# Performance work log

Measured on AMD Instinct MI355X. Metric: run time of the kernel, lower is better.

Reference implementation:

```python
import jax, jax.numpy as jnp
import numpy as np

N, E, D = 10000, 160000, 256
EPS = 1e-5


def layer_norm(x, gamma, beta):
    mu = jnp.mean(x, axis=-1, keepdims=True)
    var = jnp.var(x, axis=-1, keepdims=True)
    return (x - mu) * jax.lax.rsqrt(var + EPS) * gamma + beta


def mlp(x, w1, b1, w2, b2):
    return jax.nn.relu(x @ w1 + b1) @ w2 + b2


def setup_inputs() -> dict:
    key = jax.random.key(0)
    ks = jax.random.split(key, 16)
    s = lambda fan_in: 1.0 / np.sqrt(fan_in)
    inp = {
        'x': jax.random.normal(ks[0], (N, D), jnp.float32),
        'edge_index': jax.random.randint(ks[1], (2, E), 0, N, jnp.int64),
        'edge_attr': jax.random.normal(ks[2], (E, D), jnp.float32),
        # edge MLP: in 3D=768 -> hidden 2D=512 -> out D=256, then LN
        'e_w1': jax.random.uniform(ks[3], (3 * D, 2 * D), jnp.float32, -s(3 * D), s(3 * D)),
        'e_b1': jnp.zeros((2 * D,), jnp.float32),
        'e_w2': jax.random.uniform(ks[4], (2 * D, D), jnp.float32, -s(2 * D), s(2 * D)),
        'e_b2': jnp.zeros((D,), jnp.float32),
        'e_g': jnp.ones((D,), jnp.float32),
        'e_beta': jnp.zeros((D,), jnp.float32),
        # node MLP: in 2D=512 -> hidden 2D=512 -> out D=256, then LN
        'n_w1': jax.random.uniform(ks[5], (2 * D, 2 * D), jnp.float32, -s(2 * D), s(2 * D)),
        'n_b1': jnp.zeros((2 * D,), jnp.float32),
        'n_w2': jax.random.uniform(ks[6], (2 * D, D), jnp.float32, -s(2 * D), s(2 * D)),
        'n_b2': jnp.zeros((D,), jnp.float32),
        'n_g': jnp.ones((D,), jnp.float32),
        'n_beta': jnp.zeros((D,), jnp.float32),
    }
    return inp


def reference(x, edge_index, edge_attr, e_w1, e_b1, e_w2, e_b2, e_g, e_beta,
              n_w1, n_b1, n_w2, n_b2, n_g, n_beta):
    i, j = edge_index[0], edge_index[1]
    # Edge processor: gather, concat, MLP + LN, residual
    h = jnp.concatenate([x[i], x[j], edge_attr], axis=-1)  # [E, 3D]
    new_edge = edge_attr + layer_norm(mlp(h, e_w1, e_b1, e_w2, e_b2), e_g, e_beta)
    # Node processor: scatter-add over j, concat, MLP + LN, residual
    agg = jax.ops.segment_sum(new_edge, j, num_segments=x.shape[0])  # [N, D]
    hn = jnp.concatenate([x, agg], axis=-1)  # [N, 2D]
    new_x = x + layer_norm(mlp(hn, n_w1, n_b1, n_w2, n_b2), n_g, n_beta)
    return new_x, new_edge
```

## Files before the change

### kernel.cpp

```cpp
#include <hip/hip_runtime.h>

#define NNODE 10000
#define NEDGE 160000
#define DD 256

using f32x4  = __attribute__((ext_vector_type(4))) float;
using bf16x8 = __attribute__((ext_vector_type(8))) short;
using u32x4  = __attribute__((ext_vector_type(4))) unsigned;

__device__ inline short f2bf(float f) {
  unsigned u = __float_as_uint(f);
  unsigned r = (u + 0x7fffu + ((u >> 16) & 1u)) >> 16;
  return (short)(unsigned short)r;
}

__device__ inline unsigned pkbf(float a, float b) {
  unsigned r;
  asm("v_cvt_pk_bf16_f32 %0, %1, %2" : "=v"(r) : "v"(a), "v"(b));
  return r;
}

__global__ void cast_x_kernel(const float* __restrict__ x, short* __restrict__ xb, int total) {
  int i = blockIdx.x * 256 + threadIdx.x;
  if (i < total) xb[i] = f2bf(x[i]);
}

__global__ void pack_w_kernel(const float* __restrict__ w, short* __restrict__ p, int K, int N) {
  int idx = blockIdx.x * 256 + threadIdx.x;
  if (idx >= K * N) return;
  int k = idx / N, n = idx - k * N;
  p[(size_t)(k >> 3) * N * 8 + (size_t)n * 8 + (k & 7)] = f2bf(w[idx]);
}

__global__ void hist_kernel(const int* __restrict__ ei, int* __restrict__ deg) {
  int e = blockIdx.x * 256 + threadIdx.x;
  if (e < NEDGE) {
    int j = ei[NEDGE + e]; j = min(max(j, 0), NNODE - 1);
    atomicAdd(&deg[j], 1);
  }
}

__global__ void scan_kernel(const int* __restrict__ deg, int* __restrict__ row_start) {
  __shared__ int part[256];
  int t = threadIdx.x;
  const int CH = 40;
  int base = t * CH;
  int s = 0;
  for (int i = 0; i < CH; i++) {
    int idx = base + i;
    s += (idx < NNODE) ? deg[idx] : 0;
  }
  part[t] = s;
  __syncthreads();
  for (int off = 1; off < 256; off <<= 1) {
    int v = (t >= off) ? part[t - off] : 0;
    __syncthreads();
    part[t] += v;
    __syncthreads();
  }
  int run = (t == 0) ? 0 : part[t - 1];
  for (int i = 0; i < CH; i++) {
    int idx = base + i;
    if (idx < NNODE) { row_start[idx] = run; run += deg[idx]; }
  }
  if (t == 255) row_start[NNODE] = part[255];
}

__global__ void scatter_kernel(const int* __restrict__ ei, const int* __restrict__ row_start,
                               int* __restrict__ cursor, int* __restrict__ csr) {
  int e = blockIdx.x * 256 + threadIdx.x;
  if (e < NEDGE) {
    int j = ei[NEDGE + e]; j = min(max(j, 0), NNODE - 1);
    int p = atomicAdd(&cursor[j], 1);
    csr[row_start[j] + p] = e;
  }
}

__global__ __launch_bounds__(256) void agg_kernel(const float* __restrict__ out_e,
                                                  const int* __restrict__ row_start,
                                                  const int* __restrict__ csr,
                                                  short* __restrict__ aggb) {
  int node = blockIdx.x * 4 + (threadIdx.x >> 6);
  int lane = threadIdx.x & 63;
  if (node >= NNODE) return;
  int rs = row_start[node], re = row_start[node + 1];
  float4 acc = {0.f, 0.f, 0.f, 0.f};
  for (int k = rs; k < re; k++) {
    int eid = csr[k];
    float4 v = *(const float4*)(out_e + (size_t)eid * DD + lane * 4);
    acc.x += v.x; acc.y += v.y; acc.z += v.z; acc.w += v.w;
  }
  short4 o;
  o.x = f2bf(acc.x); o.y = f2bf(acc.y); o.z = f2bf(acc.z); o.w = f2bf(acc.w);
  *(short4*)(aggb + (size_t)node * DD + lane * 4) = o;
}

template<int MODE>
__global__ __launch_bounds__(256, 2)
void fused_mlp(const float* __restrict__ x,
               const short* __restrict__ xb,
               const int*   __restrict__ ei,
               const float* __restrict__ ea,
               const short* __restrict__ aggb,
               const short* __restrict__ w1p,
               const float* __restrict__ b1,
               const short* __restrict__ w2p,
               const float* __restrict__ b2,
               const float* __restrict__ gam,
               const float* __restrict__ bet,
               float*       __restrict__ out)
{
  constexpr int K1 = (MODE == 0) ? 768 : 512;
  constexpr int NSTEP = K1 / 64;
  constexpr int HP = 520;

  __shared__ __align__(16) short hid[64 * HP];
  __shared__ float pS[4][64];
  __shared__ float pQ[4][64];

  const int tid  = threadIdx.x;
  const int lane = tid & 63;
  const int wid  = tid >> 6;
  const int m0   = blockIdx.x * 64;
  const int lhi  = lane >> 4;
  const int llo  = lane & 15;

  const short* pI[4]; const short* pJ[4]; const float* pE[4];
  #pragma unroll
  for (int mf = 0; mf < 4; mf++) {
    int rowg = m0 + mf * 16 + llo;
    if (MODE == 0) {
      int ii = ei[rowg];         ii = min(max(ii, 0), NNODE - 1);
      int jj = ei[NEDGE + rowg]; jj = min(max(jj, 0), NNODE - 1);
      pI[mf] = xb + (size_t)ii * DD;
      pJ[mf] = xb + (size_t)jj * DD;
      pE[mf] = ea + (size_t)rowg * DD;
    } else {
      int rr = min(rowg, NNODE - 1);
      pI[mf] = xb + (size_t)rr * DD;
      pJ[mf] = aggb + (size_t)rr * DD;
      pE[mf] = nullptr;
    }
  }

  f32x4 acc1[4][8] = {};
  const bf16x8* bp1 = (const bf16x8*)w1p;
  const int bcol1 = wid * 128 + llo;

  #pragma unroll
  for (int s = 0; s < NSTEP; s++) {
    #pragma unroll
    for (int kk = 0; kk < 64; kk += 32) {
      const int ko = s * 64 + kk + lhi * 8;
      bf16x8 a[4];
      #pragma unroll
      for (int mf = 0; mf < 4; mf++) {
        if (MODE == 0) {
          if (s < 4)      a[mf] = *(const bf16x8*)(pI[mf] + ko);
          else if (s < 8) a[mf] = *(const bf16x8*)(pJ[mf] + (ko - 256));
          else {
            const float* fp = pE[mf] + (ko - 512);
            float4 u0 = *(const float4*)fp;
            float4 u1 = *(const float4*)(fp + 4);
            u32x4 q = { pkbf(u0.x, u0.y), pkbf(u0.z, u0.w),
                        pkbf(u1.x, u1.y), pkbf(u1.z, u1.w) };
            a[mf] = __builtin_bit_cast(bf16x8, q);
          }
        } else {
          if (s < 4) a[mf] = *(const bf16x8*)(pI[mf] + ko);
          else       a[mf] = *(const bf16x8*)(pJ[mf] + (ko - 256));
        }
      }
      const bf16x8* bbase = bp1 + (size_t)(((s * 64 + kk) >> 3) + lhi) * 512 + bcol1;
      #pragma unroll
      for (int nf = 0; nf < 8; nf++) {
        bf16x8 b = bbase[nf * 16];
        #pragma unroll
        for (int mf = 0; mf < 4; mf++)
          acc1[mf][nf] = __builtin_amdgcn_mfma_f32_16x16x32_bf16(a[mf], b, acc1[mf][nf], 0, 0, 0);
      }
    }
  }

  #pragma unroll
  for (int nf = 0; nf < 8; nf++) {
    int col = wid * 128 + nf * 16 + llo;
    float bb = b1[col];
    #pragma unroll
    for (int mf = 0; mf < 4; mf++) {
      #pragma unroll
      for (int r = 0; r < 4; r++) {
        float v = acc1[mf][nf][r] + bb;
        v = v > 0.f ? v : 0.f;
        hid[(mf * 16 + lhi * 4 + r) * HP + col] = f2bf(v);
      }
    }
  }
  __syncthreads();

  f32x4 acc2[4][4] = {};
  const bf16x8* bp2 = (const bf16x8*)w2p;
  const int bcol2 = wid * 64 + llo;
  #pragma unroll
  for (int kk = 0; kk < 512; kk += 32) {
    bf16x8 a[4];
    #pragma unroll
    for (int mf = 0; mf < 4; mf++)
      a[mf] = *(const bf16x8*)(hid + (mf * 16 + llo) * HP + kk + lhi * 8);
    const bf16x8* bbase = bp2 + (size_t)((kk >> 3) + lhi) * 256 + bcol2;
    #pragma unroll
    for (int nf = 0; nf < 4; nf++) {
      bf16x8 b = bbase[nf * 16];
      #pragma unroll
      for (int mf = 0; mf < 4; mf++)
        acc2[mf][nf] = __builtin_amdgcn_mfma_f32_16x16x32_bf16(a[mf], b, acc2[mf][nf], 0, 0, 0);
    }
  }

  float bb2[4], gg[4], be[4];
  #pragma unroll
  for (int nf = 0; nf < 4; nf++) {
    int col = bcol2 + nf * 16;
    bb2[nf] = b2[col]; gg[nf] = gam[col]; be[nf] = bet[col];
  }
  #pragma unroll
  for (int mf = 0; mf < 4; mf++)
    #pragma unroll
    for (int nf = 0; nf < 4; nf++)
      #pragma unroll
      for (int r = 0; r < 4; r++)
        acc2[mf][nf][r] += bb2[nf];

  float S[4][4], Q[4][4];
  #pragma unroll
  for (int mf = 0; mf < 4; mf++) {
    #pragma unroll
    for (int r = 0; r < 4; r++) {
      float s = 0.f, q = 0.f;
      #pragma unroll
      for (int nf = 0; nf < 4; nf++) {
        float v = acc2[mf][nf][r];
        s += v; q += v * v;
      }
      S[mf][r] = s; Q[mf][r] = q;
    }
  }
  #pragma unroll
  for (int m = 1; m <= 8; m <<= 1) {
    #pragma unroll
    for (int mf = 0; mf < 4; mf++)
      #pragma unroll
      for (int r = 0; r < 4; r++) {
        S[mf][r] += __shfl_xor(S[mf][r], m);
        Q[mf][r] += __shfl_xor(Q[mf][r], m);
      }
  }
  if (llo == 0) {
    #pragma unroll
    for (int mf = 0; mf < 4; mf++)
      #pragma unroll
      for (int r = 0; r < 4; r++) {
        int row = mf * 16 + lhi * 4 + r;
        pS[wid][row] = S[mf][r];
        pQ[wid][row] = Q[mf][r];
      }
  }
  __syncthreads();

  float mu[4][4], rsv[4][4];
  #pragma unroll
  for (int mf = 0; mf < 4; mf++) {
    #pragma unroll
    for (int r = 0; r < 4; r++) {
      int row = mf * 16 + lhi * 4 + r;
      float s = pS[0][row] + pS[1][row] + pS[2][row] + pS[3][row];
      float q = pQ[0][row] + pQ[1][row] + pQ[2][row] + pQ[3][row];
      float m_ = s * (1.f / 256.f);
      mu[mf][r]  = m_;
      rsv[mf][r] = rsqrtf(q * (1.f / 256.f) - m_ * m_ + 1e-5f);
    }
  }

  const float* resb = (MODE == 0) ? ea : x;
  #pragma unroll
  for (int mf = 0; mf < 4; mf++) {
    #pragma unroll
    for (int r = 0; r < 4; r++) {
      int grow = m0 + mf * 16 + lhi * 4 + r;
      if (MODE == 1 && grow >= NNODE) continue;
      const float* rp = resb + (size_t)grow * DD + bcol2;
      float*       op = out  + (size_t)grow * DD + bcol2;
      #pragma unroll
      for (int nf = 0; nf < 4; nf++) {
        float v = (acc2[mf][nf][r] - mu[mf][r]) * rsv[mf][r] * gg[nf] + be[nf] + rp[nf * 16];
        op[nf * 16] = v;
      }
    }
  }
}

extern "C" void kernel_launch(void* const* d_in, const int* in_sizes, int n_in,
                              void* d_out, int out_size, void* d_ws, size_t ws_size,
                              hipStream_t stream) {
  const float* x      = (const float*)d_in[0];
  const int*   ei     = (const int*)  d_in[1];
  const float* ea     = (const float*)d_in[2];
  const float* e_w1   = (const float*)d_in[3];
  const float* e_b1   = (const float*)d_in[4];
  const float* e_w2   = (const float*)d_in[5];
  const float* e_b2   = (const float*)d_in[6];
  const float* e_g    = (const float*)d_in[7];
  const float* e_beta = (const float*)d_in[8];
  const float* n_w1   = (const float*)d_in[9];
  const float* n_b1   = (const float*)d_in[10];
  const float* n_w2   = (const float*)d_in[11];
  const float* n_b2   = (const float*)d_in[12];
  const float* n_g    = (const float*)d_in[13];
  const float* n_beta = (const float*)d_in[14];

  float* out_x = (float*)d_out;
  float* out_e = (float*)d_out + (size_t)NNODE * DD;

  char* w = (char*)d_ws;
  short* xb   = (short*)(w);
  short* ew1p = (short*)(w + 5120000);
  short* nw1p = (short*)(w + 5906432);
  short* ew2p = (short*)(w + 6430720);
  short* nw2p = (short*)(w + 6692864);
  short* aggb = (short*)(w + 6955008);
  int*   deg  = (int*)  (w + 12075008);
  int*   cur  = (int*)  (w + 12115968);
  int*   rs   = (int*)  (w + 12156928);
  int*   csr  = (int*)  (w + 12197904);

  hipMemsetAsync(deg, 0, 81920, stream);

  cast_x_kernel<<<(NNODE * DD + 255) / 256, 256, 0, stream>>>(x, xb, NNODE * DD);
  pack_w_kernel<<<(768 * 512 + 255) / 256, 256, 0, stream>>>(e_w1, ew1p, 768, 512);
  pack_w_kernel<<<(512 * 512 + 255) / 256, 256, 0, stream>>>(n_w1, nw1p, 512, 512);
  pack_w_kernel<<<(512 * 256 + 255) / 256, 256, 0, stream>>>(e_w2, ew2p, 512, 256);
  pack_w_kernel<<<(512 * 256 + 255) / 256, 256, 0, stream>>>(n_w2, nw2p, 512, 256);

  hist_kernel<<<(NEDGE + 255) / 256, 256, 0, stream>>>(ei, deg);
  scan_kernel<<<1, 256, 0, stream>>>(deg, rs);
  scatter_kernel<<<(NEDGE + 255) / 256, 256, 0, stream>>>(ei, rs, cur, csr);

  fused_mlp<0><<<NEDGE / 64, 256, 0, stream>>>(x, xb, ei, ea, aggb,
                                               ew1p, e_b1, ew2p, e_b2, e_g, e_beta, out_e);
  agg_kernel<<<(NNODE + 3) / 4, 256, 0, stream>>>(out_e, rs, csr, aggb);
  fused_mlp<1><<<(NNODE + 63) / 64, 256, 0, stream>>>(x, xb, ei, ea, aggb,
                                                      nw1p, n_b1, nw2p, n_b2, n_g, n_beta, out_x);
}
```

Baseline: 532.6 us.

## Stage A tiles in LDS via async loads and split hidden into two halves

The fused MLP now stages the gathered activation tile into a double-buffered, XOR-swizzled LDS buffer using global_load_lds, instead of each wave loading A fragments directly from global memory. The hidden layer is computed in two 256-column halves, each fed straight into the second GEMM. This halves the acc1 registers and the hid LDS footprint, which allows raising launch bounds to 3 blocks per CU. The cost is that the first GEMM's A operand is re-staged twice and more barriers are added.

```diff
diff --git a/kernel.cpp b/kernel.cpp
--- a/kernel.cpp
+++ b/kernel.cpp
@@ -96,7 +96,7 @@
 }
 
 template<int MODE>
-__global__ __launch_bounds__(256, 2)
+__global__ __launch_bounds__(256, 3)
 void fused_mlp(const float* __restrict__ x,
                const short* __restrict__ xb,
                const int*   __restrict__ ei,
@@ -110,13 +110,14 @@
                const float* __restrict__ bet,
                float*       __restrict__ out)
 {
-  constexpr int K1 = (MODE == 0) ? 768 : 512;
-  constexpr int NSTEP = K1 / 64;
-  constexpr int HP = 520;
-
+  constexpr int K1  = (MODE == 0) ? 768 : 512;
+  constexpr int NST = K1 / 64;
+  constexpr int HP  = 264;
+
+  __shared__ __align__(16) short abuf[2][4096];
   __shared__ __align__(16) short hid[64 * HP];
-  __shared__ float pS[4][64];
-  __shared__ float pQ[4][64];
+  __shared__ int idxi[64], idxj[64];
+  __shared__ float pS[4][64], pQ[4][64];
 
   const int tid  = threadIdx.x;
   const int lane = tid & 63;
@@ -125,98 +126,140 @@
   const int lhi  = lane >> 4;
   const int llo  = lane & 15;
 
-  const short* pI[4]; const short* pJ[4]; const float* pE[4];
-  #pragma unroll
-  for (int mf = 0; mf < 4; mf++) {
-    int rowg = m0 + mf * 16 + llo;
-    if (MODE == 0) {
-      int ii = ei[rowg];         ii = min(max(ii, 0), NNODE - 1);
-      int jj = ei[NEDGE + rowg]; jj = min(max(jj, 0), NNODE - 1);
-      pI[mf] = xb + (size_t)ii * DD;
-      pJ[mf] = xb + (size_t)jj * DD;
-      pE[mf] = ea + (size_t)rowg * DD;
+  if (MODE == 0) {
+    if (tid < 64) {
+      int a = ei[m0 + tid];
+      int b = ei[NEDGE + m0 + tid];
+      idxi[tid] = min(max(a, 0), NNODE - 1);
+      idxj[tid] = min(max(b, 0), NNODE - 1);
+    }
+    __syncthreads();
+  }
+
+  const int row0 = tid >> 3;
+  const int row1 = 32 + (tid >> 3);
+  const int es0 = (((tid & 7) ^ (row0 & 7)) * 8);
+  const int es1 = (((tid & 7) ^ (row1 & 7)) * 8);
+  int offI0, offI1, offJ0, offJ1, offE0, offE1;
+  if (MODE == 0) {
+    offI0 = idxi[row0] * 512 + es0 * 2;  offI1 = idxi[row1] * 512 + es1 * 2;
+    offJ0 = idxj[row0] * 512 + es0 * 2;  offJ1 = idxj[row1] * 512 + es1 * 2;
+    offE0 = (m0 + row0) * 1024 + es0 * 4; offE1 = (m0 + row1) * 1024 + es1 * 4;
+  } else {
+    int r0 = min(m0 + row0, NNODE - 1), r1 = min(m0 + row1, NNODE - 1);
+    offI0 = r0 * 512 + es0 * 2;  offI1 = r1 * 512 + es1 * 2;
+    offJ0 = r0 * 512 + es0 * 2;  offJ1 = r1 * 512 + es1 * 2;
+    offE0 = 0; offE1 = 0;
+  }
+
+  auto STAGE = [&](int buf, int k0) {
+    if (MODE == 1 || k0 < 512) {
+      const char* base;
+      int o0, o1;
+      if (k0 < 256) {
+        base = (const char*)xb;
+        o0 = offI0 + k0 * 2; o1 = offI1 + k0 * 2;
+      } else {
+        base = (MODE == 0) ? (const char*)xb : (const char*)aggb;
+        o0 = offJ0 + (k0 - 256) * 2; o1 = offJ1 + (k0 - 256) * 2;
+      }
+      __builtin_amdgcn_global_load_lds((const int*)(base + o0),
+                                       (int*)&abuf[buf][wid * 512], 16, 0, 0);
+      __builtin_amdgcn_global_load_lds((const int*)(base + o1),
+                                       (int*)&abuf[buf][2048 + wid * 512], 16, 0, 0);
     } else {
-      int rr = min(rowg, NNODE - 1);
-      pI[mf] = xb + (size_t)rr * DD;
-      pJ[mf] = aggb + (size_t)rr * DD;
-      pE[mf] = nullptr;
-    }
-  }
-
-  f32x4 acc1[4][8] = {};
+      const char* eb = (const char*)ea;
+      const float4* f0 = (const float4*)(eb + offE0 + (k0 - 512) * 4);
+      const float4* f1 = (const float4*)(eb + offE1 + (k0 - 512) * 4);
+      float4 a0 = f0[0], a1 = f0[1];
+      float4 c0 = f1[0], c1 = f1[1];
+      u32x4 q0 = { pkbf(a0.x, a0.y), pkbf(a0.z, a0.w), pkbf(a1.x, a1.y), pkbf(a1.z, a1.w) };
+      u32x4 q1 = { pkbf(c0.x, c0.y), pkbf(c0.z, c0.w), pkbf(c1.x, c1.y), pkbf(c1.z, c1.w) };
+      *(u32x4*)&abuf[buf][tid * 8]        = q0;
+      *(u32x4*)&abuf[buf][2048 + tid * 8] = q1;
+    }
+  };
+
+  f32x4 acc1[4][4];
+  f32x4 acc2[4][4];
+  #pragma unroll
+  for (int a = 0; a < 4; a++)
+    #pragma unroll
+    for (int b = 0; b < 4; b++)
+      #pragma unroll
+      for (int r = 0; r < 4; r++) { acc1[a][b][r] = 0.f; acc2[a][b][r] = 0.f; }
+
   const bf16x8* bp1 = (const bf16x8*)w1p;
-  const int bcol1 = wid * 128 + llo;
-
-  #pragma unroll
-  for (int s = 0; s < NSTEP; s++) {
-    #pragma unroll
-    for (int kk = 0; kk < 64; kk += 32) {
-      const int ko = s * 64 + kk + lhi * 8;
-      bf16x8 a[4];
-      #pragma unroll
-      for (int mf = 0; mf < 4; mf++) {
-        if (MODE == 0) {
-          if (s < 4)      a[mf] = *(const bf16x8*)(pI[mf] + ko);
-          else if (s < 8) a[mf] = *(const bf16x8*)(pJ[mf] + (ko - 256));
-          else {
-            const float* fp = pE[mf] + (ko - 512);
-            float4 u0 = *(const float4*)fp;
-            float4 u1 = *(const float4*)(fp + 4);
-            u32x4 q = { pkbf(u0.x, u0.y), pkbf(u0.z, u0.w),
-                        pkbf(u1.x, u1.y), pkbf(u1.z, u1.w) };
-            a[mf] = __builtin_bit_cast(bf16x8, q);
-          }
-        } else {
-          if (s < 4) a[mf] = *(const bf16x8*)(pI[mf] + ko);
-          else       a[mf] = *(const bf16x8*)(pJ[mf] + (ko - 256));
-        }
-      }
-      const bf16x8* bbase = bp1 + (size_t)(((s * 64 + kk) >> 3) + lhi) * 512 + bcol1;
-      #pragma unroll
-      for (int nf = 0; nf < 8; nf++) {
-        bf16x8 b = bbase[nf * 16];
+  const bf16x8* bp2 = (const bf16x8*)w2p;
+  const int swz = llo & 7;
+
+  STAGE(0, 0);
+  __syncthreads();
+
+  #pragma unroll
+  for (int p = 0; p < 2; p++) {
+    #pragma unroll 2
+    for (int s = 0; s < NST; s++) {
+      if (s < NST - 1) STAGE((s + 1) & 1, (s + 1) * 64);
+      const short* ab = &abuf[s & 1][0];
+      #pragma unroll
+      for (int kk = 0; kk < 64; kk += 32) {
+        bf16x8 a[4];
+        const int seg = ((kk >> 3) + lhi) ^ swz;
         #pragma unroll
         for (int mf = 0; mf < 4; mf++)
-          acc1[mf][nf] = __builtin_amdgcn_mfma_f32_16x16x32_bf16(a[mf], b, acc1[mf][nf], 0, 0, 0);
-      }
-    }
-  }
-
-  #pragma unroll
-  for (int nf = 0; nf < 8; nf++) {
-    int col = wid * 128 + nf * 16 + llo;
-    float bb = b1[col];
-    #pragma unroll
-    for (int mf = 0; mf < 4; mf++) {
-      #pragma unroll
-      for (int r = 0; r < 4; r++) {
-        float v = acc1[mf][nf][r] + bb;
-        v = v > 0.f ? v : 0.f;
-        hid[(mf * 16 + lhi * 4 + r) * HP + col] = f2bf(v);
-      }
-    }
-  }
-  __syncthreads();
-
-  f32x4 acc2[4][4] = {};
-  const bf16x8* bp2 = (const bf16x8*)w2p;
+          a[mf] = *(const bf16x8*)(ab + (mf * 16 + llo) * 64 + seg * 8);
+        const bf16x8* bb = bp1 + (size_t)(s * 8 + (kk >> 3) + lhi) * 512
+                               + (p * 256 + wid * 64 + llo);
+        #pragma unroll
+        for (int nf = 0; nf < 4; nf++) {
+          bf16x8 b = bb[nf * 16];
+          #pragma unroll
+          for (int mf = 0; mf < 4; mf++)
+            acc1[mf][nf] = __builtin_amdgcn_mfma_f32_16x16x32_bf16(a[mf], b, acc1[mf][nf], 0, 0, 0);
+        }
+      }
+      __syncthreads();
+    }
+
+    #pragma unroll
+    for (int nf = 0; nf < 4; nf++) {
+      int col = wid * 64 + nf * 16 + llo;
+      float bb = b1[p * 256 + col];
+      #pragma unroll
+      for (int mf = 0; mf < 4; mf++) {
+        #pragma unroll
+        for (int r = 0; r < 4; r++) {
+          float v = acc1[mf][nf][r] + bb;
+          v = v > 0.f ? v : 0.f;
+          hid[(mf * 16 + lhi * 4 + r) * HP + col] = f2bf(v);
+          acc1[mf][nf][r] = 0.f;
+        }
+      }
+    }
+    __syncthreads();
+
+    if (p == 0) STAGE(0, 0);
+
+    #pragma unroll 2
+    for (int kk = 0; kk < 256; kk += 32) {
+      bf16x8 a[4];
+      #pragma unroll
+      for (int mf = 0; mf < 4; mf++)
+        a[mf] = *(const bf16x8*)(hid + (mf * 16 + llo) * HP + kk + lhi * 8);
+      const bf16x8* bb = bp2 + (size_t)(p * 32 + (kk >> 3) + lhi) * 256 + (wid * 64 + llo);
+      #pragma unroll
+      for (int nf = 0; nf < 4; nf++) {
+        bf16x8 b = bb[nf * 16];
+        #pragma unroll
+        for (int mf = 0; mf < 4; mf++)
+          acc2[mf][nf] = __builtin_amdgcn_mfma_f32_16x16x32_bf16(a[mf], b, acc2[mf][nf], 0, 0, 0);
+      }
+    }
+    __syncthreads();
+  }
+
   const int bcol2 = wid * 64 + llo;
-  #pragma unroll
-  for (int kk = 0; kk < 512; kk += 32) {
-    bf16x8 a[4];
-    #pragma unroll
-    for (int mf = 0; mf < 4; mf++)
-      a[mf] = *(const bf16x8*)(hid + (mf * 16 + llo) * HP + kk + lhi * 8);
-    const bf16x8* bbase = bp2 + (size_t)((kk >> 3) + lhi) * 256 + bcol2;
-    #pragma unroll
-    for (int nf = 0; nf < 4; nf++) {
-      bf16x8 b = bbase[nf * 16];
-      #pragma unroll
-      for (int mf = 0; mf < 4; mf++)
-        acc2[mf][nf] = __builtin_amdgcn_mfma_f32_16x16x32_bf16(a[mf], b, acc2[mf][nf], 0, 0, 0);
-    }
-  }
-
   float bb2[4], gg[4], be[4];
   #pragma unroll
   for (int nf = 0; nf < 4; nf++) {
```

Result: slower. 546.4 us (+2.6%).

## Precompute per-node first-layer projections and gather them per edge

Applied to the files above, without the earlier changes.

The first edge-MLP layer is split algebraically: x@W1a and x@W1b are computed once per node (10k rows) into a bf16 table, and each edge gathers two 512-wide rows and adds them to edge_attr@W1c. This cuts the edge GEMM K dimension from 768 to 256. It removes the redundant per-edge recomputation of node projections. Edge_attr is now staged through LDS with an XOR swizzle, and the hidden buffer is swizzled too. The cost is an extra bf16 rounding of the partial sums, a 20MB intermediate, and random gathers of 1KB rows per edge.

```diff
diff --git a/kernel.cpp b/kernel.cpp
--- a/kernel.cpp
+++ b/kernel.cpp
@@ -12,6 +12,10 @@
   unsigned u = __float_as_uint(f);
   unsigned r = (u + 0x7fffu + ((u >> 16) & 1u)) >> 16;
   return (short)(unsigned short)r;
+}
+
+__device__ inline float bf2f(short s) {
+  return __uint_as_float(((unsigned)(unsigned short)s) << 16);
 }
 
 __device__ inline unsigned pkbf(float a, float b) {
@@ -30,6 +34,23 @@
   if (idx >= K * N) return;
   int k = idx / N, n = idx - k * N;
   p[(size_t)(k >> 3) * N * 8 + (size_t)n * 8 + (k & 7)] = f2bf(w[idx]);
+}
+
+__global__ void pack_ew1_kernel(const float* __restrict__ w, short* __restrict__ w1abp,
+                                short* __restrict__ w1cp) {
+  int idx = blockIdx.x * 256 + threadIdx.x;
+  if (idx >= 768 * 512) return;
+  int k = idx >> 9, n = idx & 511;
+  short v = f2bf(w[idx]);
+  if (k < 256) {
+    w1abp[(size_t)(k >> 3) * 1024 * 8 + (size_t)n * 8 + (k & 7)] = v;
+  } else if (k < 512) {
+    int kk = k - 256;
+    w1abp[(size_t)(kk >> 3) * 1024 * 8 + (size_t)(512 + n) * 8 + (kk & 7)] = v;
+  } else {
+    int kk = k - 512;
+    w1cp[(size_t)(kk >> 3) * 512 * 8 + (size_t)n * 8 + (kk & 7)] = v;
+  }
 }
 
 __global__ void hist_kernel(const int* __restrict__ ei, int* __restrict__ deg) {
@@ -95,28 +116,284 @@
   *(short4*)(aggb + (size_t)node * DD + lane * 4) = o;
 }
 
-template<int MODE>
 __global__ __launch_bounds__(256, 2)
-void fused_mlp(const float* __restrict__ x,
-               const short* __restrict__ xb,
-               const int*   __restrict__ ei,
-               const float* __restrict__ ea,
-               const short* __restrict__ aggb,
-               const short* __restrict__ w1p,
-               const float* __restrict__ b1,
-               const short* __restrict__ w2p,
-               const float* __restrict__ b2,
-               const float* __restrict__ gam,
-               const float* __restrict__ bet,
-               float*       __restrict__ out)
+void precomp_pab(const short* __restrict__ xb, const short* __restrict__ w1abp,
+                 short* __restrict__ pab) {
+  __shared__ __align__(16) short abuf[2048 * 8];
+
+  const int tid  = threadIdx.x;
+  const int lane = tid & 63;
+  const int wid  = tid >> 6;
+  const int lhi  = lane >> 4;
+  const int llo  = lane & 15;
+  const int swz  = llo & 7;
+  const int m0   = blockIdx.x * 64;
+  const int h    = blockIdx.y;
+
+  #pragma unroll
+  for (int q = 0; q < 8; q++) {
+    int S = wid * 512 + q * 64 + lane;
+    int row = S >> 5;
+    int segp = S & 31;
+    int seg = segp ^ (row & 7);
+    int rowg = min(m0 + row, NNODE - 1);
+    __builtin_amdgcn_global_load_lds(
+        (const int*)((const char*)xb + (size_t)rowg * 512 + seg * 16),
+        (int*)(abuf + (size_t)(wid * 512 + q * 64) * 8), 16, 0, 0);
+  }
+  __syncthreads();
+
+  f32x4 acc1[4][8] = {};
+  const bf16x8* bp1 = (const bf16x8*)w1abp;
+  #pragma unroll
+  for (int kk = 0; kk < 256; kk += 32) {
+    const int ks = kk >> 3;
+    bf16x8 a[4];
+    #pragma unroll
+    for (int mf = 0; mf < 4; mf++)
+      a[mf] = *(const bf16x8*)(abuf + ((mf * 16 + llo) * 32 + ((ks + lhi) ^ swz)) * 8);
+    const bf16x8* bb = bp1 + (size_t)(ks + lhi) * 1024 + h * 512 + wid * 128 + llo;
+    #pragma unroll
+    for (int nf = 0; nf < 8; nf++) {
+      bf16x8 b = bb[nf * 16];
+      #pragma unroll
+      for (int mf = 0; mf < 4; mf++)
+        acc1[mf][nf] = __builtin_amdgcn_mfma_f32_16x16x32_bf16(a[mf], b, acc1[mf][nf], 0, 0, 0);
+    }
+  }
+
+  #pragma unroll
+  for (int mf = 0; mf < 4; mf++) {
+    #pragma unroll
+    for (int r = 0; r < 4; r++) {
+      int row = m0 + mf * 16 + lhi * 4 + r;
+      if (row < NNODE) {
+        u32x4 wv = { pkbf(acc1[mf][0][r], acc1[mf][1][r]),
+                     pkbf(acc1[mf][2][r], acc1[mf][3][r]),
+                     pkbf(acc1[mf][4][r], acc1[mf][5][r]),
+                     pkbf(acc1[mf][6][r], acc1[mf][7][r]) };
+        *(u32x4*)(pab + (size_t)row * 1024 + h * 512 + llo * 32 + wid * 8) = wv;
+      }
+    }
+  }
+}
+
+__global__ __launch_bounds__(256, 2)
+void fused_edge(const int* __restrict__ ei,
+                const float* __restrict__ ea,
+                const short* __restrict__ pab,
+                const short* __restrict__ w1cp,
+                const float* __restrict__ b1,
+                const short* __restrict__ w2p,
+                const float* __restrict__ b2,
+                const float* __restrict__ gam,
+                const float* __restrict__ bet,
+                float* __restrict__ out)
 {
-  constexpr int K1 = (MODE == 0) ? 768 : 512;
-  constexpr int NSTEP = K1 / 64;
+  __shared__ __align__(16) short hid[64 * 512];
+  __shared__ int idxi[64], idxj[64];
+  __shared__ float pS[256], pQ[256];
+
+  short* abuf = hid;
+
+  const int tid  = threadIdx.x;
+  const int lane = tid & 63;
+  const int wid  = tid >> 6;
+  const int lhi  = lane >> 4;
+  const int llo  = lane & 15;
+  const int swz  = llo & 7;
+  const int m0   = blockIdx.x * 64;
+
+  if (tid < 64) {
+    int a = ei[m0 + tid];
+    int b = ei[NEDGE + m0 + tid];
+    idxi[tid] = min(max(a, 0), NNODE - 1);
+    idxj[tid] = min(max(b, 0), NNODE - 1);
+  }
+
+  #pragma unroll
+  for (int q = 0; q < 8; q++) {
+    int S = q * 256 + tid;
+    int row = S >> 5;
+    int segp = S & 31;
+    int seg = segp ^ (row & 7);
+    const float* src = ea + (size_t)(m0 + row) * 256 + seg * 8;
+    float4 u0 = *(const float4*)src;
+    float4 u1 = *(const float4*)(src + 4);
+    u32x4 qv = { pkbf(u0.x, u0.y), pkbf(u0.z, u0.w), pkbf(u1.x, u1.y), pkbf(u1.z, u1.w) };
+    *(u32x4*)(abuf + (size_t)S * 8) = qv;
+  }
+  __syncthreads();
+
+  f32x4 acc1[4][8] = {};
+  const bf16x8* bp1 = (const bf16x8*)w1cp;
+  #pragma unroll
+  for (int kk = 0; kk < 256; kk += 32) {
+    const int ks = kk >> 3;
+    bf16x8 a[4];
+    #pragma unroll
+    for (int mf = 0; mf < 4; mf++)
+      a[mf] = *(const bf16x8*)(abuf + ((mf * 16 + llo) * 32 + ((ks + lhi) ^ swz)) * 8);
+    const bf16x8* bb = bp1 + (size_t)(ks + lhi) * 512 + wid * 128 + llo;
+    #pragma unroll
+    for (int nf = 0; nf < 8; nf++) {
+      bf16x8 b = bb[nf * 16];
+      #pragma unroll
+      for (int mf = 0; mf < 4; mf++)
+        acc1[mf][nf] = __builtin_amdgcn_mfma_f32_16x16x32_bf16(a[mf], b, acc1[mf][nf], 0, 0, 0);
+    }
+  }
+
+  #pragma unroll
+  for (int mf = 0; mf < 4; mf++) {
+    #pragma unroll
+    for (int r = 0; r < 4; r++) {
+      int row = mf * 16 + lhi * 4 + r;
+      int gi = idxi[row], gj = idxj[row];
+      bf16x8 pa = *(const bf16x8*)(pab + (size_t)gi * 1024 + llo * 32 + wid * 8);
+      bf16x8 pb = *(const bf16x8*)(pab + (size_t)gj * 1024 + 512 + llo * 32 + wid * 8);
+      #pragma unroll
+      for (int nf = 0; nf < 8; nf++)
+        acc1[mf][nf][r] += bf2f(pa[nf]) + bf2f(pb[nf]);
+    }
+  }
+  __syncthreads();
+
+  #pragma unroll
+  for (int nf = 0; nf < 8; nf++) {
+    int col = wid * 128 + nf * 16 + llo;
+    float bb = b1[col];
+    int cs = col >> 3, cl = col & 7;
+    #pragma unroll
+    for (int mf = 0; mf < 4; mf++) {
+      #pragma unroll
+      for (int r = 0; r < 4; r++) {
+        int row = mf * 16 + lhi * 4 + r;
+        float v = acc1[mf][nf][r] + bb;
+        v = v > 0.f ? v : 0.f;
+        hid[row * 512 + ((cs ^ (row & 7)) * 8) + cl] = f2bf(v);
+      }
+    }
+  }
+  __syncthreads();
+
+  f32x4 acc2[4][4] = {};
+  const bf16x8* bp2 = (const bf16x8*)w2p;
+  const int bcol2 = wid * 64 + llo;
+  #pragma unroll
+  for (int kk = 0; kk < 512; kk += 32) {
+    const int ks = kk >> 3;
+    bf16x8 a[4];
+    #pragma unroll
+    for (int mf = 0; mf < 4; mf++) {
+      int row = mf * 16 + llo;
+      a[mf] = *(const bf16x8*)(hid + row * 512 + (((ks + lhi) ^ swz) * 8));
+    }
+    const bf16x8* bb = bp2 + (size_t)(ks + lhi) * 256 + bcol2;
+    #pragma unroll
+    for (int nf = 0; nf < 4; nf++) {
+      bf16x8 b = bb[nf * 16];
+      #pragma unroll
+      for (int mf = 0; mf < 4; mf++)
+        acc2[mf][nf] = __builtin_amdgcn_mfma_f32_16x16x32_bf16(a[mf], b, acc2[mf][nf], 0, 0, 0);
+    }
+  }
+
+  float bb2[4], gg[4], be[4];
+  #pragma unroll
+  for (int nf = 0; nf < 4; nf++) {
+    int col = bcol2 + nf * 16;
+    bb2[nf] = b2[col]; gg[nf] = gam[col]; be[nf] = bet[col];
+  }
+  #pragma unroll
+  for (int mf = 0; mf < 4; mf++)
+    #pragma unroll
+    for (int nf = 0; nf < 4; nf++)
+      #pragma unroll
+      for (int r = 0; r < 4; r++)
+        acc2[mf][nf][r] += bb2[nf];
+
+  float S[4][4], Q[4][4];
+  #pragma unroll
+  for (int mf = 0; mf < 4; mf++) {
+    #pragma unroll
+    for (int r = 0; r < 4; r++) {
+      float s = 0.f, q = 0.f;
+      #pragma unroll
+      for (int nf = 0; nf < 4; nf++) {
+        float v = acc2[mf][nf][r];
+        s += v; q += v * v;
+      }
+      S[mf][r] = s; Q[mf][r] = q;
+    }
+  }
+  #pragma unroll
+  for (int m = 1; m <= 8; m <<= 1) {
+    #pragma unroll
+    for (int mf = 0; mf < 4; mf++)
+      #pragma unroll
+      for (int r = 0; r < 4; r++) {
+        S[mf][r] += __shfl_xor(S[mf][r], m);
+        Q[mf][r] += __shfl_xor(Q[mf][r], m);
+      }
+  }
+  if (llo == 0) {
+    #pragma unroll
+    for (int mf = 0; mf < 4; mf++)
+      #pragma unroll
+      for (int r = 0; r < 4; r++) {
+        int row = mf * 16 + lhi * 4 + r;
+        pS[wid * 64 + row] = S[mf][r];
+        pQ[wid * 64 + row] = Q[mf][r];
+      }
+  }
+  __syncthreads();
+
+  float mu[4][4], rsv[4][4];
+  #pragma unroll
+  for (int mf = 0; mf < 4; mf++) {
+    #pragma unroll
+    for (int r = 0; r < 4; r++) {
+      int row = mf * 16 + lhi * 4 + r;
+      float s = pS[row] + pS[64 + row] + pS[128 + row] + pS[192 + row];
+      float q = pQ[row] + pQ[64 + row] + pQ[128 + row] + pQ[192 + row];
+      float m_ = s * (1.f / 256.f);
+      mu[mf][r]  = m_;
+      rsv[mf][r] = rsqrtf(q * (1.f / 256.f) - m_ * m_ + 1e-5f);
+    }
+  }
+
+  #pragma unroll
+  for (int mf = 0; mf < 4; mf++) {
+    #pragma unroll
+    for (int r = 0; r < 4; r++) {
+      int grow = m0 + mf * 16 + lhi * 4 + r;
+      const float* rp = ea  + (size_t)grow * DD + bcol2;
+      float*       op = out + (size_t)grow * DD + bcol2;
+      #pragma unroll
+      for (int nf = 0; nf < 4; nf++) {
+        float v = (acc2[mf][nf][r] - mu[mf][r]) * rsv[mf][r] * gg[nf] + be[nf] + rp[nf * 16];
+        op[nf * 16] = v;
+      }
+    }
+  }
+}
+
+__global__ __launch_bounds__(256, 2)
+void fused_node(const float* __restrict__ x,
+                const short* __restrict__ xb,
+                const short* __restrict__ aggb,
+                const short* __restrict__ w1p,
+                const float* __restrict__ b1,
+                const short* __restrict__ w2p,
+                const float* __restrict__ b2,
+                const float* __restrict__ gam,
+                const float* __restrict__ bet,
+                float* __restrict__ out)
+{
   constexpr int HP = 520;
-
   __shared__ __align__(16) short hid[64 * HP];
-  __shared__ float pS[4][64];
-  __shared__ float pQ[4][64];
+  __shared__ float pS[4][64], pQ[4][64];
 
   const int tid  = threadIdx.x;
   const int lane = tid & 63;
@@ -125,22 +402,12 @@
   const int lhi  = lane >> 4;
   const int llo  = lane & 15;
 
-  const short* pI[4]; const short* pJ[4]; const float* pE[4];
-  #pragma unroll
-  for (int mf = 0; mf < 4; mf++) {
-    int rowg = m0 + mf * 16 + llo;
-    if (MODE == 0) {
-      int ii = ei[rowg];         ii = min(max(ii, 0), NNODE - 1);
-      int jj = ei[NEDGE + rowg]; jj = min(max(jj, 0), NNODE - 1);
-      pI[mf] = xb + (size_t)ii * DD;
-      pJ[mf] = xb + (size_t)jj * DD;
-      pE[mf] = ea + (size_t)rowg * DD;
-    } else {
-      int rr = min(rowg, NNODE - 1);
-      pI[mf] = xb + (size_t)rr * DD;
-      pJ[mf] = aggb + (size_t)rr * DD;
-      pE[mf] = nullptr;
-    }
+  const short* pI[4]; const short* pJ[4];
+  #pragma unroll
+  for (int mf = 0; mf < 4; mf++) {
+    int rr = min(m0 + mf * 16 + llo, NNODE - 1);
+    pI[mf] = xb + (size_t)rr * DD;
+    pJ[mf] = aggb + (size_t)rr * DD;
   }
 
   f32x4 acc1[4][8] = {};
@@ -148,33 +415,20 @@
   const int bcol1 = wid * 128 + llo;
 
   #pragma unroll
-  for (int s = 0; s < NSTEP; s++) {
+  for (int s = 0; s < 8; s++) {
     #pragma unroll
     for (int kk = 0; kk < 64; kk += 32) {
       const int ko = s * 64 + kk + lhi * 8;
       bf16x8 a[4];
       #pragma unroll
       for (int mf = 0; mf < 4; mf++) {
-        if (MODE == 0) {
-          if (s < 4)      a[mf] = *(const bf16x8*)(pI[mf] + ko);
-          else if (s < 8) a[mf] = *(const bf16x8*)(pJ[mf] + (ko - 256));
-          else {
-            const float* fp = pE[mf] + (ko - 512);
-            float4 u0 = *(const float4*)fp;
-            float4 u1 = *(const float4*)(fp + 4);
-            u32x4 q = { pkbf(u0.x, u0.y), pkbf(u0.z, u0.w),
-                        pkbf(u1.x, u1.y), pkbf(u1.z, u1.w) };
-            a[mf] = __builtin_bit_cast(bf16x8, q);
-          }
-        } else {
-          if (s < 4) a[mf] = *(const bf16x8*)(pI[mf] + ko);
-          else       a[mf] = *(const bf16x8*)(pJ[mf] + (ko - 256));
-        }
-      }
-      const bf16x8* bbase = bp1 + (size_t)(((s * 64 + kk) >> 3) + lhi) * 512 + bcol1;
+        if (s < 4) a[mf] = *(const bf16x8*)(pI[mf] + ko);
+        else       a[mf] = *(const bf16x8*)(pJ[mf] + (ko - 256));
+      }
+      const bf16x8* bb = bp1 + (size_t)(s * 8 + (kk >> 3) + lhi) * 512 + bcol1;
       #pragma unroll
       for (int nf = 0; nf < 8; nf++) {
-        bf16x8 b = bbase[nf * 16];
+        bf16x8 b = bb[nf * 16];
         #pragma unroll
         for (int mf = 0; mf < 4; mf++)
           acc1[mf][nf] = __builtin_amdgcn_mfma_f32_16x16x32_bf16(a[mf], b, acc1[mf][nf], 0, 0, 0);
@@ -207,10 +461,10 @@
     #pragma unroll
     for (int mf = 0; mf < 4; mf++)
       a[mf] = *(const bf16x8*)(hid + (mf * 16 + llo) * HP + kk + lhi * 8);
-    const bf16x8* bbase = bp2 + (size_t)((kk >> 3) + lhi) * 256 + bcol2;
+    const bf16x8* bb = bp2 + (size_t)((kk >> 3) + lhi) * 256 + bcol2;
     #pragma unroll
     for (int nf = 0; nf < 4; nf++) {
-      bf16x8 b = bbase[nf * 16];
+      bf16x8 b = bb[nf * 16];
       #pragma unroll
       for (int mf = 0; mf < 4; mf++)
         acc2[mf][nf] = __builtin_amdgcn_mfma_f32_16x16x32_bf16(a[mf], b, acc2[mf][nf], 0, 0, 0);
@@ -281,15 +535,14 @@
     }
   }
 
-  const float* resb = (MODE == 0) ? ea : x;
   #pragma unroll
   for (int mf = 0; mf < 4; mf++) {
     #pragma unroll
     for (int r = 0; r < 4; r++) {
       int grow = m0 + mf * 16 + lhi * 4 + r;
-      if (MODE == 1 && grow >= NNODE) continue;
-      const float* rp = resb + (size_t)grow * DD + bcol2;
-      float*       op = out  + (size_t)grow * DD + bcol2;
+      if (grow >= NNODE) continue;
+      const float* rp = x   + (size_t)grow * DD + bcol2;
+      float*       op = out + (size_t)grow * DD + bcol2;
       #pragma unroll
       for (int nf = 0; nf < 4; nf++) {
         float v = (acc2[mf][nf][r] - mu[mf][r]) * rsv[mf][r] * gg[nf] + be[nf] + rp[nf * 16];
@@ -322,21 +575,23 @@
   float* out_e = (float*)d_out + (size_t)NNODE * DD;
 
   char* w = (char*)d_ws;
-  short* xb   = (short*)(w);
-  short* ew1p = (short*)(w + 5120000);
-  short* nw1p = (short*)(w + 5906432);
-  short* ew2p = (short*)(w + 6430720);
-  short* nw2p = (short*)(w + 6692864);
-  short* aggb = (short*)(w + 6955008);
-  int*   deg  = (int*)  (w + 12075008);
-  int*   cur  = (int*)  (w + 12115968);
-  int*   rs   = (int*)  (w + 12156928);
-  int*   csr  = (int*)  (w + 12197904);
+  short* xb    = (short*)(w);
+  short* aggb  = (short*)(w + 5120000);
+  short* pab   = (short*)(w + 10240000);
+  short* w1abp = (short*)(w + 30720000);
+  short* w1cp  = (short*)(w + 31244288);
+  short* ew2p  = (short*)(w + 31506432);
+  short* nw1p  = (short*)(w + 31768576);
+  short* nw2p  = (short*)(w + 32292864);
+  int*   deg   = (int*)  (w + 32555008);
+  int*   cur   = (int*)  (w + 32595968);
+  int*   rs    = (int*)  (w + 32636928);
+  int*   csr   = (int*)  (w + 32677904);
 
   hipMemsetAsync(deg, 0, 81920, stream);
 
   cast_x_kernel<<<(NNODE * DD + 255) / 256, 256, 0, stream>>>(x, xb, NNODE * DD);
-  pack_w_kernel<<<(768 * 512 + 255) / 256, 256, 0, stream>>>(e_w1, ew1p, 768, 512);
+  pack_ew1_kernel<<<(768 * 512 + 255) / 256, 256, 0, stream>>>(e_w1, w1abp, w1cp);
   pack_w_kernel<<<(512 * 512 + 255) / 256, 256, 0, stream>>>(n_w1, nw1p, 512, 512);
   pack_w_kernel<<<(512 * 256 + 255) / 256, 256, 0, stream>>>(e_w2, ew2p, 512, 256);
   pack_w_kernel<<<(512 * 256 + 255) / 256, 256, 0, stream>>>(n_w2, nw2p, 512, 256);
@@ -345,9 +600,11 @@
   scan_kernel<<<1, 256, 0, stream>>>(deg, rs);
   scatter_kernel<<<(NEDGE + 255) / 256, 256, 0, stream>>>(ei, rs, cur, csr);
 
-  fused_mlp<0><<<NEDGE / 64, 256, 0, stream>>>(x, xb, ei, ea, aggb,
-                                               ew1p, e_b1, ew2p, e_b2, e_g, e_beta, out_e);
+  precomp_pab<<<dim3((NNODE + 63) / 64, 2), 256, 0, stream>>>(xb, w1abp, pab);
+
+  fused_edge<<<NEDGE / 64, 256, 0, stream>>>(ei, ea, pab, w1cp, e_b1,
+                                             ew2p, e_b2, e_g, e_beta, out_e);
   agg_kernel<<<(NNODE + 3) / 4, 256, 0, stream>>>(out_e, rs, csr, aggb);
-  fused_mlp<1><<<(NNODE + 63) / 64, 256, 0, stream>>>(x, xb, ei, ea, aggb,
-                                                      nw1p, n_b1, nw2p, n_b2, n_g, n_beta, out_x);
-}
+  fused_node<<<(NNODE + 63) / 64, 256, 0, stream>>>(x, xb, aggb, nw1p, n_b1,
+                                                    nw2p, n_b2, n_g, n_beta, out_x);
+}
```

New measurement: 532.1 us. Within noise of the previous version (-0.1%).
